# Optimization experiments

Hardware: AMD Instinct MI355X
Metric: run time of the kernel (lower is better)

## Reference

```python
import jax, jax.numpy as jnp
import numpy as np

FEAT_STRIDE = 16
PRE_NMS = 6000
POST_NMS = 300
NMS_THRESH = 0.7
NEG_THR = 0.3
POS_THR = 0.7
RPN_BATCH = 256
FG_FRAC = 0.5
SCALES = (8, 16, 32)
RATIOS = (0.5, 1.0, 2.0)
A = len(SCALES) * len(RATIOS)  # 9


def _generate_anchors():
    base = 16.0
    ctr = (base - 1.0) * 0.5
    size = base * base
    out = []
    for r in RATIOS:
        ws = np.round(np.sqrt(size / r))
        hs = np.round(ws * r)
        for s in SCALES:
            W = ws * s
            H = hs * s
            out.append([ctr - 0.5 * (W - 1), ctr - 0.5 * (H - 1),
                        ctr + 0.5 * (W - 1), ctr + 0.5 * (H - 1)])
    return np.array(out, np.float32)  # [9,4]


def _conv(x, w, b, pad):
    y = jax.lax.conv_general_dilated(x, w, (1, 1), [(pad, pad), (pad, pad)],
                                     dimension_numbers=('NCHW', 'OIHW', 'NCHW'))
    return y + b[None, :, None, None]


def _all_anchors(H, W):
    base = jnp.asarray(_generate_anchors())
    sx = jnp.arange(W, dtype=jnp.float32) * FEAT_STRIDE
    sy = jnp.arange(H, dtype=jnp.float32) * FEAT_STRIDE
    gy, gx = jnp.meshgrid(sy, sx, indexing='ij')
    shifts = jnp.stack([gx, gy, gx, gy], -1).reshape(-1, 1, 4)  # [H*W,1,4]
    return (shifts + base[None]).reshape(-1, 4)  # (h,w,a) order, [H*W*A,4]


def _decode(anchors, deltas):
    w = anchors[:, 2] - anchors[:, 0] + 1.0
    h = anchors[:, 3] - anchors[:, 1] + 1.0
    cx = anchors[:, 0] + 0.5 * w
    cy = anchors[:, 1] + 0.5 * h
    pcx = deltas[:, 0] * w + cx
    pcy = deltas[:, 1] * h + cy
    pw = jnp.exp(deltas[:, 2]) * w
    ph = jnp.exp(deltas[:, 3]) * h
    return jnp.stack([pcx - 0.5 * pw, pcy - 0.5 * ph, pcx + 0.5 * pw, pcy + 0.5 * ph], -1)


def _encode(anchors, gt):
    ew = anchors[:, 2] - anchors[:, 0] + 1.0
    eh = anchors[:, 3] - anchors[:, 1] + 1.0
    ecx = anchors[:, 0] + 0.5 * ew
    ecy = anchors[:, 1] + 0.5 * eh
    gw = gt[:, 2] - gt[:, 0] + 1.0
    gh = gt[:, 3] - gt[:, 1] + 1.0
    gcx = gt[:, 0] + 0.5 * gw
    gcy = gt[:, 1] + 0.5 * gh
    return jnp.stack([(gcx - ecx) / ew, (gcy - ecy) / eh,
                      jnp.log(gw / ew), jnp.log(gh / eh)], -1)


def _nms(boxes, scores, thresh, max_out):
    x1, y1, x2, y2 = boxes[:, 0], boxes[:, 1], boxes[:, 2], boxes[:, 3]
    areas = (x2 - x1 + 1.0) * (y2 - y1 + 1.0)
    N = boxes.shape[0]

    def body(k, st):
        valid, sel, selv = st
        s = jnp.where(valid, scores, -jnp.inf)
        i = jnp.argmax(s)
        ok = s[i] > -jnp.inf
        iw = jnp.maximum(jnp.minimum(x2[i], x2) - jnp.maximum(x1[i], x1) + 1.0, 0.0)
        ih = jnp.maximum(jnp.minimum(y2[i], y2) - jnp.maximum(y1[i], y1) + 1.0, 0.0)
        inter = iw * ih
        iou = inter / (areas[i] + areas - inter)
        valid = valid & (iou <= thresh)
        return valid, sel.at[k].set(i.astype(jnp.int32)), selv.at[k].set(ok)

    st = jax.lax.fori_loop(0, max_out, body,
                           (jnp.ones(N, bool), jnp.zeros(max_out, jnp.int32), jnp.zeros(max_out, bool)))
    return st[1], st[2]


def _propose_one(scores, deltas, anchors, imh, imw):
    boxes = _decode(anchors, deltas)
    boxes = jnp.stack([jnp.clip(boxes[:, 0], 0.0, imw - 1.0),
                       jnp.clip(boxes[:, 1], 0.0, imh - 1.0),
                       jnp.clip(boxes[:, 2], 0.0, imw - 1.0),
                       jnp.clip(boxes[:, 3], 0.0, imh - 1.0)], -1)
    top_s, idx = jax.lax.top_k(scores, PRE_NMS)
    top_b = boxes[idx]
    sel, selv = _nms(top_b, top_s, NMS_THRESH, POST_NMS)
    return top_b[sel] * selv[:, None].astype(top_b.dtype)  # [POST_NMS,4], zero rows when exhausted


def _anchor_target_one(gt, imh, imw, rfg, rbg, anchors):
    N = anchors.shape[0]
    ax1, ay1, ax2, ay2 = anchors[:, 0], anchors[:, 1], anchors[:, 2], anchors[:, 3]
    inside = (ax1 >= 0) & (ay1 >= 0) & (ax2 < imw) & (ay2 < imh)
    gx1, gy1, gx2, gy2 = gt[:, 0], gt[:, 1], gt[:, 2], gt[:, 3]
    gw = gx2 - gx1 + 1.0
    gh = gy2 - gy1 + 1.0
    gt_valid = ~((gw == 1.0) & (gh == 1.0))  # all-zero padded gt boxes
    aw = ax2 - ax1 + 1.0
    ah = ay2 - ay1 + 1.0
    iw = jnp.maximum(jnp.minimum(ax2[:, None], gx2[None, :]) - jnp.maximum(ax1[:, None], gx1[None, :]) + 1.0, 0.0)
    ih = jnp.maximum(jnp.minimum(ay2[:, None], gy2[None, :]) - jnp.maximum(ay1[:, None], gy1[None, :]) + 1.0, 0.0)
    inter = iw * ih
    iou = inter / ((aw * ah)[:, None] + (gw * gh)[None, :] - inter)  # [N,K]
    iou = jnp.where(gt_valid[None, :], iou, 0.0)
    iou = jnp.where(inside[:, None], iou, -1.0)  # outside anchors excluded, as in original
    max_ov = iou.max(1)
    arg = iou.argmax(1)
    gt_max = iou.max(0)
    gt_max = jnp.where(gt_max <= 0.0, 1e-5, gt_max)
    keep = (iou == gt_max[None, :]).any(1)  # anchors with max overlap per gt -> fg
    labels = jnp.full(N, -1.0, jnp.float32)
    labels = jnp.where(max_ov < NEG_THR, 0.0, labels)
    labels = jnp.where(keep, 1.0, labels)
    labels = jnp.where(max_ov >= POS_THR, 1.0, labels)
    labels = jnp.where(inside, labels, -1.0)

    def ranks(r, mask):
        order = jnp.argsort(jnp.where(mask, r, 2.0))
        return jnp.zeros(N, jnp.int32).at[order].set(jnp.arange(N, dtype=jnp.int32))

    num_fg = int(FG_FRAC * RPN_BATCH)
    fg_keep = (labels == 1.0) & (ranks(rfg, labels == 1.0) < num_fg)
    num_bg = RPN_BATCH - fg_keep.sum()
    bg_keep = (labels == 0.0) & (ranks(rbg, labels == 0.0) < num_bg)
    labels = jnp.where(fg_keep, 1.0, jnp.where(bg_keep, 0.0, -1.0))
    targets = _encode(anchors, gt[arg, :4])
    ones4 = jnp.ones((1, 4), jnp.float32)
    in_w = (labels == 1.0).astype(jnp.float32)[:, None] * ones4
    n_ex = (labels >= 0).sum().astype(jnp.float32)
    out_w = jnp.where(labels >= 0, 1.0 / n_ex, 0.0)[:, None] * ones4
    return labels, targets, in_w, out_w


def _rpn_forward(base_feat, im_info, gt_boxes, conv_w, conv_b, cls_w, cls_b, bbox_w, bbox_b):
    B, _, H, W = base_feat.shape
    x = jax.nn.relu(_conv(base_feat, conv_w, conv_b, 1))
    cls_score = _conv(x, cls_w, cls_b, 0)                 # [B,2A,H,W]
    # reshape(x,2) -> softmax over axis 1 -> reshape back
    prob = jax.nn.softmax(cls_score.reshape(B, 2, A * H, W), axis=1).reshape(B, 2 * A, H, W)
    bbox_pred = _conv(x, bbox_w, bbox_b, 0)               # [B,4A,H,W]
    anchors = _all_anchors(H, W)                          # [H*W*A,4]

    # ---- proposal layer (detached in original) ----
    fg = prob[:, A:, :, :].transpose(0, 2, 3, 1).reshape(B, -1)        # (h,w,a)
    deltas = bbox_pred.transpose(0, 2, 3, 1).reshape(B, -1, 4)
    rois_boxes = jax.vmap(_propose_one, in_axes=(0, 0, None, 0, 0))(
        jax.lax.stop_gradient(fg), jax.lax.stop_gradient(deltas), anchors, im_info[:, 0], im_info[:, 1])
    batch_idx = jnp.broadcast_to(jnp.arange(B, dtype=rois_boxes.dtype)[:, None, None], (B, POST_NMS, 1))
    rois = jnp.concatenate([batch_idx, rois_boxes], -1)   # [B,POST_NMS,5]

    # ---- anchor target layer (training path) ----
    key = jax.random.key(42)
    rfg = jax.random.uniform(key, (B, anchors.shape[0]))
    rbg = jax.random.uniform(jax.random.fold_in(key, 1), (B, anchors.shape[0]))
    labels, targets, in_w, out_w = jax.vmap(_anchor_target_one, in_axes=(0, 0, 0, 0, 0, None))(
        gt_boxes, im_info[:, 0], im_info[:, 1], rfg, rbg, anchors)
    # rearrange (h,w,a) -> (a,h,w) layouts to match torch permutes
    labels = labels.reshape(B, H, W, A).transpose(0, 3, 1, 2).reshape(B, -1)
    targets = targets.reshape(B, H, W, A * 4).transpose(0, 3, 1, 2)
    in_w = in_w.reshape(B, H, W, A * 4).transpose(0, 3, 1, 2)
    out_w = out_w.reshape(B, H, W, A * 4).transpose(0, 3, 1, 2)

    # cross-entropy over kept anchors
    logits = cls_score.reshape(B, 2, A, H, W).transpose(0, 2, 3, 4, 1).reshape(-1, 2)
    lab = labels.reshape(-1)
    m = (lab >= 0).astype(logits.dtype)
    logp = jax.nn.log_softmax(logits, axis=-1)
    idx = jnp.clip(lab, 0.0, 1.0).astype(jnp.int32)
    nll = -jnp.take_along_axis(logp, idx[:, None], axis=1)[:, 0]
    loss_cls = (nll * m).sum() / m.sum()

    # smooth-L1 box loss, sigma=3, sum dims [1,2,3] then mean over batch
    sigma2 = 9.0
    diff = in_w * (bbox_pred - targets)
    ad = jnp.abs(diff)
    flag = (ad < 1.0 / sigma2).astype(diff.dtype)
    lb = flag * 0.5 * sigma2 * diff * diff + (1.0 - flag) * (ad - 0.5 / sigma2)
    loss_box = (out_w * lb).sum(axis=(1, 2, 3)).mean()
    return rois, loss_cls, loss_box


def setup_inputs() -> dict:
    key = jax.random.key(0)
    ks = jax.random.split(key, 9)
    B, C, H, W = 4, 512, 50, 76
    base_feat = jax.random.normal(ks[0], (B, C, H, W), jnp.float32)
    conv_w = jax.random.normal(ks[1], (512, C, 3, 3), jnp.float32) * 0.01
    conv_b = jnp.zeros((512,), jnp.float32)
    cls_w = jax.random.normal(ks[2], (18, 512, 1, 1), jnp.float32) * 0.01
    cls_b = jnp.zeros((18,), jnp.float32)
    bbox_w = jax.random.normal(ks[3], (36, 512, 1, 1), jnp.float32) * 0.01
    bbox_b = jnp.zeros((36,), jnp.float32)
    imh, imw = float(H * FEAT_STRIDE), float(W * FEAT_STRIDE)
    im_info = jnp.tile(jnp.array([imh, imw, 1.0], jnp.float32), (B, 1))
    K = 20
    cx = jax.random.uniform(ks[4], (B, K)) * (imw - 100.0) + 50.0
    cy = jax.random.uniform(ks[5], (B, K)) * (imh - 100.0) + 50.0
    bw = jax.random.uniform(ks[6], (B, K)) * 270.0 + 30.0
    bh = jax.random.uniform(ks[7], (B, K)) * 270.0 + 30.0
    x1 = jnp.clip(cx - 0.5 * bw, 0.0, imw - 1.0)
    x2 = jnp.clip(cx + 0.5 * bw, 0.0, imw - 1.0)
    y1 = jnp.clip(cy - 0.5 * bh, 0.0, imh - 1.0)
    y2 = jnp.clip(cy + 0.5 * bh, 0.0, imh - 1.0)
    cls = jax.random.randint(ks[8], (B, K), 1, 21).astype(jnp.float32)
    gt_boxes = jnp.stack([x1, y1, x2, y2, cls], -1)
    num_boxes = jnp.full((B,), K, jnp.int32)
    return {"base_feat": base_feat, "im_info": im_info, "gt_boxes": gt_boxes,
            "num_boxes": num_boxes, "conv_w": conv_w, "conv_b": conv_b,
            "cls_w": cls_w, "cls_b": cls_b, "bbox_w": bbox_w, "bbox_b": bbox_b}


def reference(base_feat, im_info, gt_boxes, num_boxes, conv_w, conv_b, cls_w, cls_b, bbox_w, bbox_b):
    # num_boxes is implicitly handled via zero-padded gt_boxes (as in the original layer)
    return _rpn_forward(base_feat, im_info, gt_boxes, conv_w, conv_b, cls_w, cls_b, bbox_w, bbox_b)
```

## Files before the change

### kernel.cpp

```cpp
#include <hip/hip_runtime.h>
#include <stdint.h>

#define HHH 50
#define WWW 76
#define NPIX 3800
#define NA 34200
#define PRE 6000
#define POST 300
#define NW 94
#define CIN 512
#define COUT 512
#define NBATCH 4
#define NGT 20
#define TFHALF 68400u
#define XTB 2252800

typedef __bf16 bf16x8 __attribute__((ext_vector_type(8)));
typedef float f32x4 __attribute__((ext_vector_type(4)));
typedef unsigned int u32x4v __attribute__((ext_vector_type(4)));

__device__ static inline f32x4 MFMA16(bf16x8 a, bf16x8 b, f32x4 c) {
  return __builtin_amdgcn_mfma_f32_16x16x32_bf16(a, b, c, 0, 0, 0);
}
__device__ static inline bf16x8 LD8(const unsigned short* p) {
  return __builtin_bit_cast(bf16x8, *(const u32x4v*)p);
}

__host__ __device__ static inline void tf2x32(unsigned k0, unsigned k1, unsigned& x0, unsigned& x1) {
  unsigned k2 = k0 ^ k1 ^ 0x1BD11BDAu;
#define TFR(r) do { x0 += x1; x1 = (x1 << (r)) | (x1 >> (32 - (r))); x1 ^= x0; } while (0)
  x0 += k0; x1 += k1;
  TFR(13); TFR(15); TFR(26); TFR(6);
  x0 += k1; x1 += k2 + 1u;
  TFR(17); TFR(29); TFR(16); TFR(24);
  x0 += k2; x1 += k0 + 2u;
  TFR(13); TFR(15); TFR(26); TFR(6);
  x0 += k0; x1 += k1 + 3u;
  TFR(17); TFR(29); TFR(16); TFR(24);
  x0 += k1; x1 += k2 + 4u;
  TFR(13); TFR(15); TFR(26); TFR(6);
  x0 += k2; x1 += k0 + 5u;
#undef TFR
}

__device__ static inline unsigned tf_u23(unsigned k0, unsigned k1, unsigned p) {
  unsigned x0, x1;
  if (p < TFHALF) { x0 = p; x1 = p + TFHALF; tf2x32(k0, k1, x0, x1); return x0 >> 9; }
  x0 = p - TFHALF; x1 = p; tf2x32(k0, k1, x0, x1); return x1 >> 9;
}

__device__ const float BA[9][4] = {
  {-84.f, -40.f,  99.f,  55.f}, {-176.f, -88.f, 191.f, 103.f}, {-360.f, -184.f, 375.f, 199.f},
  {-56.f, -56.f,  71.f,  71.f}, {-120.f, -120.f, 135.f, 135.f}, {-248.f, -248.f, 263.f, 263.f},
  {-36.f, -80.f,  51.f,  95.f}, {-80.f, -168.f,  95.f, 183.f}, {-168.f, -344.f, 183.f, 359.f}
};

__device__ static inline unsigned monoF(float f) {
  int b = __float_as_int(f);
  unsigned u = (unsigned)b;
  return (b < 0) ? ~u : (u | 0x80000000u);
}
__device__ static inline float unmonoF(unsigned u) {
  unsigned b = (u & 0x80000000u) ? (u ^ 0x80000000u) : ~u;
  return __int_as_float((int)b);
}

__device__ static inline void split3(float v, unsigned short& h, unsigned short& m, unsigned short& l) {
  __bf16 b0 = (__bf16)v;  float f0 = (float)b0;
  float r = v - f0;       __bf16 b1 = (__bf16)r;  float f1 = (float)b1;
  float r2 = r - f1;      __bf16 b2 = (__bf16)r2;
  h = __builtin_bit_cast(unsigned short, b0);
  m = __builtin_bit_cast(unsigned short, b1);
  l = __builtin_bit_cast(unsigned short, b2);
}

__global__ void k_split_x(const float* __restrict__ feat, unsigned short* __restrict__ x0,
                          unsigned short* __restrict__ x1, unsigned short* __restrict__ x2) {
  int tid = blockIdx.x * 256 + threadIdx.x;
  if (tid >= NBATCH * XTB) return;
  int b = tid / XTB;
  int rem = tid - b * XTB;
  int pg = rem >> 13;
  int r2 = rem & 8191;
  int cg = r2 >> 7;
  int po = (r2 >> 3) & 15;
  int cl = r2 & 7;
  int ci = cg * 8 + cl;
  int px = pg * 16 + po;
  int hq = px / 80, wq = px - hq * 80;
  float v = 0.f;
  if (hq >= 2 && hq < 52 && wq >= 1 && wq < 77)
    v = feat[((size_t)(b * 512 + ci)) * NPIX + (hq - 2) * 76 + (wq - 1)];
  unsigned short h, m, l;
  split3(v, h, m, l);
  x0[tid] = h; x1[tid] = m; x2[tid] = l;
}

__global__ void k_split_w(const float* __restrict__ cw, unsigned short* __restrict__ w0,
                          unsigned short* __restrict__ w1, unsigned short* __restrict__ w2,
                          unsigned* __restrict__ gtmaxU, int* __restrict__ cnts, float* __restrict__ accums) {
  int tid = blockIdx.x * 256 + threadIdx.x;
  if (blockIdx.x == 0) {
    int t = threadIdx.x;
    if (t < NBATCH * NGT) gtmaxU[t] = 0x407FFFFFu;
    if (t < 8) cnts[t] = 0;
    if (t < 8) accums[t] = 0.f;
  }
  if (tid >= 9 * 64 * 512 * 8) return;
  int cl = tid & 7;
  int co = (tid >> 3) & 511;
  int cg = (tid >> 12) & 63;
  int tap = tid >> 18;
  int ci = cg * 8 + cl;
  float v = cw[((size_t)co * 512 + ci) * 9 + tap];
  unsigned short h, m, l;
  split3(v, h, m, l);
  w0[tid] = h; w1[tid] = m; w2[tid] = l;
}

__global__ void k_tr_w1(const float* __restrict__ clsw, const float* __restrict__ bbw, float* __restrict__ wt1) {
  int tid = blockIdx.x * 256 + threadIdx.x;
  if (tid >= CIN * 64) return;
  int c = tid & 63, ci = tid >> 6;
  float v = 0.f;
  if (c < 18) v = clsw[c * 512 + ci];
  else if (c < 54) v = bbw[(c - 18) * 512 + ci];
  wt1[tid] = v;
}

__global__ __launch_bounds__(256, 2) void k_conv3(
    const unsigned short* __restrict__ XT0, const unsigned short* __restrict__ XT1,
    const unsigned short* __restrict__ XT2,
    const unsigned short* __restrict__ WT0, const unsigned short* __restrict__ WT1,
    const unsigned short* __restrict__ WT2,
    const float* __restrict__ bias, float* __restrict__ out) {
  const int d = blockIdx.x;
  const int copair = (d >> 1) & 3, half = d & 1, g = d >> 3;
  const int cob = copair * 2 + (g & 1);
  const int pxb = half * 64 + (g >> 1);
  const int pxp = pxb & 31, b = pxb >> 5;
  const int co0 = cob * 64;
  const int px0 = 160 + pxp * 128;
  const int t = threadIdx.x, l = t & 63, wv = t >> 6;
  const int wr = wv >> 1, wc = wv & 1;
  const int l15 = l & 15, lq = l >> 4;
  f32x4 cmain[2][4], ccorr[2][4];
  double accd[2][4][4];
#pragma unroll
  for (int c = 0; c < 2; ++c)
#pragma unroll
    for (int p = 0; p < 4; ++p) {
      cmain[c][p] = (f32x4)(0.f); ccorr[c][p] = (f32x4)(0.f);
#pragma unroll
      for (int r = 0; r < 4; ++r) accd[c][p][r] = 0.0;
    }
  const unsigned short* xt0 = XT0 + (size_t)b * XTB;
  const unsigned short* xt1 = XT1 + (size_t)b * XTB;
  const unsigned short* xt2 = XT2 + (size_t)b * XTB;
  const int coA = wr * 32 + l15;
  const int OFFT[9] = {-81, -80, -79, -1, 0, 1, 79, 80, 81};
  const int pxw = px0 + wc * 64 + l15;

  for (int kg = 0; kg < 16; ++kg) {
    const int cgl = kg * 4 + lq;
    const int cglo = cgl * 128;
    const size_t aro = ((size_t)cgl * 512 + co0 + coA) * 8;
#pragma unroll
    for (int tap = 0; tap < 9; ++tap) {
      const size_t ao = aro + (size_t)tap * (64 * 512 * 8);
      bf16x8 A0[2], A1[2], A2[2];
      A0[0] = LD8(WT0 + ao); A0[1] = LD8(WT0 + ao + 128);
      A1[0] = LD8(WT1 + ao); A1[1] = LD8(WT1 + ao + 128);
      A2[0] = LD8(WT2 + ao); A2[1] = LD8(WT2 + ao + 128);
      const int pxbase = pxw + OFFT[tap];
      const size_t eob = (size_t)((pxbase >> 4) * 8192 + (pxbase & 15) * 8 + cglo);
#pragma unroll
      for (int p = 0; p < 4; ++p) {
        const size_t eo = eob + (size_t)p * 8192;
        bf16x8 B0 = LD8(xt0 + eo);
        bf16x8 B1 = LD8(xt1 + eo);
        bf16x8 B2 = LD8(xt2 + eo);
#pragma unroll
        for (int c = 0; c < 2; ++c) {
          cmain[c][p] = MFMA16(A0[c], B0, cmain[c][p]);
          ccorr[c][p] = MFMA16(A2[c], B0, ccorr[c][p]);
          ccorr[c][p] = MFMA16(A0[c], B2, ccorr[c][p]);
          ccorr[c][p] = MFMA16(A1[c], B1, ccorr[c][p]);
          ccorr[c][p] = MFMA16(A1[c], B0, ccorr[c][p]);
          ccorr[c][p] = MFMA16(A0[c], B1, ccorr[c][p]);
        }
      }
    }
    if (kg & 1) {
#pragma unroll
      for (int c = 0; c < 2; ++c)
#pragma unroll
        for (int p = 0; p < 4; ++p) {
#pragma unroll
          for (int r = 0; r < 4; ++r) accd[c][p][r] += (double)cmain[c][p][r];
          cmain[c][p] = (f32x4)(0.f);
        }
    }
  }
  const size_t outb = ((size_t)b * 512 + co0) * NPIX;
#pragma unroll
  for (int c = 0; c < 2; ++c)
#pragma unroll
    for (int p = 0; p < 4; ++p)
#pragma unroll
      for (int r = 0; r < 4; ++r) {
        int coL = wr * 32 + c * 16 + lq * 4 + r;
        int px = px0 + wc * 64 + p * 16 + l15;
        int hq = px / 80, wq = px - hq * 80;
        if (hq >= 2 && hq < 52 && wq >= 1 && wq < 77) {
          float v = (float)(accd[c][p][r] + (double)ccorr[c][p][r]) + bias[co0 + coL];
          out[outb + (size_t)coL * NPIX + (hq - 2) * 76 + (wq - 1)] = fmaxf(v, 0.f);
        }
      }
}

__global__ __launch_bounds__(256) void k_conv1(const float* __restrict__ x, const float* __restrict__ wt1,
                                               const float* __restrict__ clsb, const float* __restrict__ bbb,
                                               float* __restrict__ clsS, float* __restrict__ bbp) {
  const int b = blockIdx.y;
  const int px0 = blockIdx.x * 128;
  const int t = threadIdx.x;
  const int cg = t & 7, pg = t >> 3;
  __shared__ float xs[16][128];
  __shared__ float ws[16][72];
  double acc[8][4];
#pragma unroll
  for (int i = 0; i < 8; ++i)
#pragma unroll
    for (int j = 0; j < 4; ++j) acc[i][j] = 0.0;
  const float* xb = x + (size_t)b * CIN * NPIX;
  for (int cc = 0; cc < CIN; cc += 16) {
#pragma unroll
    for (int e0 = 0; e0 < 8; ++e0) {
      int e = t + e0 * 256;
      int r = e >> 7, c = e & 127;
      int p = px0 + c;
      xs[r][c] = (p < NPIX) ? xb[(size_t)(cc + r) * NPIX + p] : 0.f;
    }
#pragma unroll
    for (int e0 = 0; e0 < 4; ++e0) {
      int e = t + e0 * 256;
      int r = e >> 6, c = e & 63;
      ws[r][c + ((c >> 5) << 2)] = wt1[(cc + r) * 64 + c];
    }
    __syncthreads();
    const int wcol = (cg << 3) + ((cg >> 2) << 2);
    const int xcol = pg << 2;
    float a32[8][4];
#pragma unroll
    for (int i = 0; i < 8; ++i)
#pragma unroll
      for (int j = 0; j < 4; ++j) a32[i][j] = 0.f;
#pragma unroll
    for (int k = 0; k < 16; ++k) {
      const float4 w0 = *(const float4*)&ws[k][wcol];
      const float4 w1 = *(const float4*)&ws[k][wcol + 4];
      const float4 xa = *(const float4*)&xs[k][xcol];
      const float wv[8] = {w0.x, w0.y, w0.z, w0.w, w1.x, w1.y, w1.z, w1.w};
      const float xv[4] = {xa.x, xa.y, xa.z, xa.w};
#pragma unroll
      for (int i = 0; i < 8; ++i)
#pragma unroll
        for (int j = 0; j < 4; ++j)
          a32[i][j] = fmaf(wv[i], xv[j], a32[i][j]);
    }
#pragma unroll
    for (int i = 0; i < 8; ++i)
#pragma unroll
      for (int j = 0; j < 4; ++j) acc[i][j] += (double)a32[i][j];
    __syncthreads();
  }
#pragma unroll
  for (int i = 0; i < 8; ++i) {
    int c = cg * 8 + i;
#pragma unroll
    for (int j = 0; j < 4; ++j) {
      int p = px0 + pg * 4 + j;
      if (p < NPIX) {
        if (c < 18) clsS[((size_t)b * 18 + c) * NPIX + p] = (float)acc[i][j] + clsb[c];
        else if (c < 54) bbp[((size_t)b * 36 + (c - 18)) * NPIX + p] = (float)acc[i][j] + bbb[c - 18];
      }
    }
  }
}

__global__ void k_decode(const float* __restrict__ clsS, const float* __restrict__ bbp,
                         const float* __restrict__ im_info, float* __restrict__ boxes,
                         unsigned long long* __restrict__ keys) {
  int tid = blockIdx.x * 256 + threadIdx.x;
  int b = tid >> 16, n = tid & 0xFFFF;
  if (n >= NA) return;
  int a = n % 9, p = n / 9;
  int h = p / WWW, w = p - h * WWW;
  const float* cb = clsS + (size_t)b * 18 * NPIX;
  float s0 = cb[(size_t)a * NPIX + p];
  float s1 = cb[(size_t)(9 + a) * NPIX + p];
  float mx = fmaxf(s0, s1);
  float e0 = expf(s0 - mx), e1 = expf(s1 - mx);
  float fg = e1 / (e0 + e1);
  const float* bb = bbp + (size_t)b * 36 * NPIX;
  float d0 = bb[(size_t)(a * 4 + 0) * NPIX + p];
  float d1 = bb[(size_t)(a * 4 + 1) * NPIX + p];
  float d2 = bb[(size_t)(a * 4 + 2) * NPIX + p];
  float d3 = bb[(size_t)(a * 4 + 3) * NPIX + p];
  float ax1 = BA[a][0] + w * 16.f, ay1 = BA[a][1] + h * 16.f;
  float ax2 = BA[a][2] + w * 16.f, ay2 = BA[a][3] + h * 16.f;
  float aw = ax2 - ax1 + 1.f, ah = ay2 - ay1 + 1.f;
  float acx = ax1 + 0.5f * aw, acy = ay1 + 0.5f * ah;
  float pcx = d0 * aw + acx, pcy = d1 * ah + acy;
  float pw = expf(d2) * aw, ph = expf(d3) * ah;
  float imh = im_info[b * 3 + 0], imw = im_info[b * 3 + 1];
  float x1 = fminf(fmaxf(pcx - 0.5f * pw, 0.f), imw - 1.f);
  float y1 = fminf(fmaxf(pcy - 0.5f * ph, 0.f), imh - 1.f);
  float x2 = fminf(fmaxf(pcx + 0.5f * pw, 0.f), imw - 1.f);
  float y2 = fminf(fmaxf(pcy + 0.5f * ph, 0.f), imh - 1.f);
  float* bx = boxes + ((size_t)b * NA + n) * 4;
  bx[0] = x1; bx[1] = y1; bx[2] = x2; bx[3] = y2;
  unsigned fb = __float_as_uint(fg);
  keys[((size_t)b << 16) + n] = ((unsigned long long)fb << 32) | (unsigned)(~(unsigned)n);
}

__global__ __launch_bounds__(1024) void k_rsel_top(const unsigned long long* __restrict__ keys,
                                                   unsigned long long* __restrict__ comp) {
  const int b = blockIdx.x;
  const unsigned long long* kb = keys + ((size_t)b << 16);
  __shared__ int hist[16][256];
  __shared__ int histT[256];
  __shared__ unsigned long long sh_prefix;
  __shared__ unsigned sh_r;
  __shared__ int sh_cnt;
  const int t = threadIdx.x, wid = t >> 6, lane = t & 63;
  if (t == 0) { sh_prefix = 0ull; sh_r = PRE; sh_cnt = 0; }
  __syncthreads();
  for (int p = 5; p >= 0; --p) {
    for (int e = t; e < 4096; e += 1024) ((int*)hist)[e] = 0;
    __syncthreads();
    unsigned long long pref = sh_prefix;
    for (int i = t; i < NA; i += 1024) {
      unsigned long long k = kb[i];
      unsigned long long k48 = ((k >> 16) & 0xFFFFFFFF0000ull) | (k & 0xFFFFull);
      bool m = (p == 5) || ((k48 >> (8 * (p + 1))) == pref);
      unsigned bucket = (unsigned)((k48 >> (8 * p)) & 255);
      unsigned long long act = __ballot(m);
      while (act) {
        int src = __ffsll(act) - 1;
        unsigned v0 = __shfl(bucket, src);
        unsigned long long same = __ballot(m && (bucket == v0));
        if (lane == src) atomicAdd(&hist[wid][v0], (int)__popcll(same));
        act &= ~same;
      }
    }
    __syncthreads();
    if (t < 256) { int s = 0; for (int w = 0; w < 16; ++w) s += hist[w][t]; histT[t] = s; }
    __syncthreads();
    if (t == 0) {
      unsigned rr = sh_r; unsigned cum = 0;
      for (int v = 255; v >= 0; --v) {
        cum += (unsigned)histT[v];
        if (cum >= rr) { sh_r = rr - (cum - (unsigned)histT[v]); sh_prefix = (sh_prefix << 8) | (unsigned)v; break; }
      }
    }
    __syncthreads();
  }
  const unsigned long long thr48 = sh_prefix;
  for (int base = 0; base < NA; base += 1024) {
    int i = base + t;
    bool keep = false;
    unsigned long long k = 0ull;
    if (i < NA) {
      k = kb[i];
      unsigned long long k48 = ((k >> 16) & 0xFFFFFFFF0000ull) | (k & 0xFFFFull);
      keep = (k48 >= thr48);
    }
    unsigned long long bal = __ballot(keep);
    if (bal) {
      int leader = __ffsll(bal) - 1;
      int basepos = 0;
      if (lane == leader) basepos = atomicAdd(&sh_cnt, (int)__popcll(bal));
      basepos = __shfl(basepos, leader);
      if (keep) {
        int off = __popcll(bal & ((1ull << lane) - 1ull));
        comp[b * 8192 + basepos + off] = k;
      }
    }
  }
}

__global__ __launch_bounds__(1024) void k_sort_lds(unsigned long long* __restrict__ comp) {
  __shared__ unsigned long long s[8192];
  const int b = blockIdx.x;
  const int t = threadIdx.x;
  unsigned long long* cb = comp + b * 8192;
  for (int e = t; e < 8192; e += 1024) s[e] = (e < PRE) ? cb[e] : 0ull;
  __syncthreads();
  for (int k = 2; k <= 8192; k <<= 1) {
    for (int j = k >> 1; j >= 1; j >>= 1) {
      for (int q = t; q < 4096; q += 1024) {
        int i = ((q & ~(j - 1)) << 1) | (q & (j - 1));
        int pp = i | j;
        bool up = (i & k) == 0;
        unsigned long long a = s[i], d = s[pp];
        if (up ? (a < d) : (a > d)) { s[i] = d; s[pp] = a; }
      }
      __syncthreads();
    }
  }
  for (int e = t; e < PRE; e += 1024) cb[e] = s[e];
}

__global__ void k_gather(const unsigned long long* __restrict__ comp, const float* __restrict__ boxes,
                         float* tbx1, float* tby1, float* tbx2, float* tby2, float* tba) {
  int tid = blockIdx.x * 256 + threadIdx.x;
  if (tid >= NBATCH * PRE) return;
  int b = tid / PRE;
  int k = tid - b * PRE;
  unsigned long long key = comp[b * 8192 + k];
  unsigned n = ~(unsigned)(key & 0xFFFFFFFFu);
  const float* bx = boxes + ((size_t)b * NA + n) * 4;
  float x1 = bx[0], y1 = bx[1], x2 = bx[2], y2 = bx[3];
  tbx1[tid] = x1; tby1[tid] = y1; tbx2[tid] = x2; tby2[tid] = y2;
  tba[tid] = (x2 - x1 + 1.f) * (y2 - y1 + 1.f);
}

__global__ __launch_bounds__(256) void k_mask(const float* __restrict__ tbx1, const float* __restrict__ tby1,
                                              const float* __restrict__ tbx2, const float* __restrict__ tby2,
                                              const float* __restrict__ tba, unsigned long long* __restrict__ mask) {
  const int b = blockIdx.y;
  const int i0 = blockIdx.x * 64;
  const int t = threadIdx.x;
  __shared__ float jx1[2048], jy1[2048], jx2[2048], jy2[2048], ja[2048];
  __shared__ float ix1[64], iy1[64], ix2[64], iy2[64], ia[64];
  const float* bx1 = tbx1 + b * PRE;
  const float* by1 = tby1 + b * PRE;
  const float* bx2 = tbx2 + b * PRE;
  const float* by2 = tby2 + b * PRE;
  const float* ba2 = tba + b * PRE;
  if (t < 64) {
    int i = i0 + t;
    if (i < PRE) { ix1[t] = bx1[i]; iy1[t] = by1[i]; ix2[t] = bx2[i]; iy2[t] = by2[i]; ia[t] = ba2[i]; }
    else { ix1[t] = 0; iy1[t] = 0; ix2[t] = 0; iy2[t] = 0; ia[t] = 1; }
  }
  for (int c = 0; c < 3; ++c) {
    int j0 = c * 2048;
    for (int e = t; e < 2048; e += 256) {
      int j = j0 + e;
      if (j < PRE) { jx1[e] = bx1[j]; jy1[e] = by1[j]; jx2[e] = bx2[j]; jy2[e] = by2[j]; ja[e] = ba2[j]; }
      else { jx1[e] = 0; jy1[e] = 0; jx2[e] = 0; jy2[e] = 0; ja[e] = 1; }
    }
    __syncthreads();
    for (int task = t; task < 64 * 32; task += 256) {
      int il = task & 63, wl = task >> 6;
      int i = i0 + il;
      int wg = (j0 >> 6) + wl;
      if (i >= PRE || wg >= NW) continue;
      unsigned long long word = 0ull;
      float X1 = ix1[il], Y1 = iy1[il], X2 = ix2[il], Y2 = iy2[il], A = ia[il];
      for (int l = 0; l < 64; ++l) {
        int j = wg * 64 + l;
        if (j > i && j < PRE) {
          int e = j - j0;
          float iw = fminf(X2, jx2[e]) - fmaxf(X1, jx1[e]) + 1.f;
          float ih = fminf(Y2, jy2[e]) - fmaxf(Y1, jy1[e]) + 1.f;
          if (iw > 0.f && ih > 0.f) {
            float inter = iw * ih;
            float iou = inter / (A + ja[e] - inter);
            if (iou > 0.7f) word |= (1ull << l);
          }
        }
      }
      mask[((size_t)(b * PRE + i)) * NW + wg] = word;
    }
    __syncthreads();
  }
}

__global__ void k_nms(const unsigned long long* __restrict__ mask,
                      const float* __restrict__ tbx1, const float* __restrict__ tby1,
                      const float* __restrict__ tbx2, const float* __restrict__ tby2,
                      float* __restrict__ out) {
  const int b = blockIdx.x;
  const int lane = threadIdx.x;
  unsigned long long rem0 = 0ull;
  unsigned long long rem1;
  if (64 + lane < NW) rem1 = (64 + lane == NW - 1) ? ~((1ull << (PRE - (NW - 1) * 64)) - 1ull) : 0ull;
  else rem1 = ~0ull;
  int sc = 0;
  for (; sc < POST; ++sc) {
    unsigned long long a0 = ~rem0, a1 = ~rem1;
    unsigned long long bal0 = __ballot(a0 != 0ull);
    int w, l;
    if (bal0) {
      int src = __ffsll(bal0) - 1;
      unsigned long long av = __shfl(a0, src);
      w = src; l = __ffsll(av) - 1;
    } else {
      unsigned long long bal1 = __ballot(a1 != 0ull);
      if (!bal1) break;
      int src = __ffsll(bal1) - 1;
      unsigned long long av = __shfl(a1, src);
      w = 64 + src; l = __ffsll(av) - 1;
    }
    int j = w * 64 + l;
    if (lane < 5) {
      float v;
      if (lane == 0) v = (float)b;
      else if (lane == 1) v = tbx1[b * PRE + j];
      else if (lane == 2) v = tby1[b * PRE + j];
      else if (lane == 3) v = tbx2[b * PRE + j];
      else v = tby2[b * PRE + j];
      out[((size_t)(b * POST + sc)) * 5 + lane] = v;
    }
    const unsigned long long* row = mask + ((size_t)(b * PRE + j)) * NW;
    rem0 |= row[lane];
    if (64 + lane < NW) rem1 |= row[64 + lane];
    if (w < 64) { if (lane == w) rem0 |= (1ull << l); }
    else if (lane == w - 64) rem1 |= (1ull << l);
  }
  for (int r2 = sc; r2 < POST; ++r2)
    if (lane < 5) out[((size_t)(b * POST + r2)) * 5 + lane] = (lane == 0) ? (float)b : 0.f;
}

__global__ __launch_bounds__(256) void k_iouA(const float* __restrict__ gt_boxes, const float* __restrict__ im_info,
                                              float* __restrict__ iou, float* __restrict__ maxov,
                                              int* __restrict__ argm, unsigned* __restrict__ gtmaxU) {
  const int b = blockIdx.y;
  const int n = blockIdx.x * 256 + threadIdx.x;
  __shared__ float g[NGT][6];
  if (threadIdx.x < NGT) {
    const float* gg = gt_boxes + (b * NGT + threadIdx.x) * 5;
    float x1 = gg[0], y1 = gg[1], x2 = gg[2], y2 = gg[3];
    g[threadIdx.x][0] = x1; g[threadIdx.x][1] = y1; g[threadIdx.x][2] = x2; g[threadIdx.x][3] = y2;
    float gw = x2 - x1 + 1.f, gh = y2 - y1 + 1.f;
    g[threadIdx.x][4] = gw * gh;
    g[threadIdx.x][5] = ((gw == 1.f) && (gh == 1.f)) ? 0.f : 1.f;
  }
  __syncthreads();
  if (n >= NA) return;
  int a = n % 9, p = n / 9;
  int h = p / WWW, w = p - h * WWW;
  float ax1 = BA[a][0] + w * 16.f, ay1 = BA[a][1] + h * 16.f;
  float ax2 = BA[a][2] + w * 16.f, ay2 = BA[a][3] + h * 16.f;
  float imh = im_info[b * 3 + 0], imw = im_info[b * 3 + 1];
  bool inside = (ax1 >= 0.f) && (ay1 >= 0.f) && (ax2 < imw) && (ay2 < imh);
  float aw = ax2 - ax1 + 1.f, ah = ay2 - ay1 + 1.f;
  float aa = aw * ah;
  float best = -2.f;
  int barg = 0;
  float* row = iou + ((size_t)(b * NA) + n) * NGT;
#pragma unroll
  for (int j = 0; j < NGT; ++j) {
    float iw = fmaxf(fminf(ax2, g[j][2]) - fmaxf(ax1, g[j][0]) + 1.f, 0.f);
    float ih = fmaxf(fminf(ay2, g[j][3]) - fmaxf(ay1, g[j][1]) + 1.f, 0.f);
    float inter = iw * ih;
    float v = inter / (aa + g[j][4] - inter);
    if (g[j][5] == 0.f) v = 0.f;
    if (!inside) v = -1.f;
    row[j] = v;
    if (v > best) { best = v; barg = j; }
    if (v > 0.f) atomicMax(&gtmaxU[b * NGT + j], monoF(v));
  }
  maxov[b * NA + n] = best;
  argm[b * NA + n] = barg;
}

__global__ __launch_bounds__(256) void k_labels(const float* __restrict__ iou, const float* __restrict__ maxov,
                                                const unsigned* __restrict__ gtmaxU, const float* __restrict__ im_info,
                                                unsigned kf0, unsigned kf1, unsigned kb0, unsigned kb1,
                                                int* __restrict__ labels, unsigned* __restrict__ ufg,
                                                unsigned* __restrict__ ubg, int* __restrict__ cnts) {
  const int b = blockIdx.y;
  const int n = blockIdx.x * 256 + threadIdx.x;
  __shared__ float gmf[NGT];
  if (threadIdx.x < NGT) {
    float gm = unmonoF(gtmaxU[b * NGT + threadIdx.x]);
    gmf[threadIdx.x] = (gm <= 0.f) ? 1e-5f : gm;
  }
  __syncthreads();
  int label = -1;
  if (n < NA) {
    int a = n % 9, p = n / 9;
    int h = p / WWW, w = p - h * WWW;
    float ax1 = BA[a][0] + w * 16.f, ay1 = BA[a][1] + h * 16.f;
    float ax2 = BA[a][2] + w * 16.f, ay2 = BA[a][3] + h * 16.f;
    float imh = im_info[b * 3 + 0], imw = im_info[b * 3 + 1];
    bool inside = (ax1 >= 0.f) && (ay1 >= 0.f) && (ax2 < imw) && (ay2 < imh);
    float mo = maxov[b * NA + n];
    const float* row = iou + ((size_t)(b * NA) + n) * NGT;
    bool keep = false;
#pragma unroll
    for (int j = 0; j < NGT; ++j) keep = keep || (row[j] == gmf[j]);
    if (mo < 0.3f) label = 0;
    if (keep) label = 1;
    if (mo >= 0.7f) label = 1;
    if (!inside) label = -1;
    labels[b * NA + n] = label;
    unsigned pp = (unsigned)(b * NA + n);
    ufg[b * NA + n] = (label == 1) ? tf_u23(kf0, kf1, pp) : 0x00FFFFFFu;
    ubg[b * NA + n] = (label == 0) ? tf_u23(kb0, kb1, pp) : 0x00FFFFFFu;
  }
  unsigned long long bf = __ballot(label == 1);
  unsigned long long bb = __ballot(label == 0);
  if ((threadIdx.x & 63) == 0) {
    atomicAdd(&cnts[b], (int)__popcll(bf));
    atomicAdd(&cnts[4 + b], (int)__popcll(bb));
  }
}

__global__ __launch_bounds__(1024) void k_rsel_samp(const unsigned* __restrict__ ufg, const unsigned* __restrict__ ubg,
                                                    const int* __restrict__ cnts, unsigned* __restrict__ selp,
                                                    float* __restrict__ nexf) {
  const int blk = blockIdx.x;
  const int b = blk >> 1, cls = blk & 1;
  const unsigned* u = (cls == 0 ? ufg : ubg) + (size_t)b * NA;
  const int fcnt = cnts[b], bcnt = cnts[4 + b];
  const int kk = (cls == 0) ? 128 : (256 - (fcnt < 128 ? fcnt : 128));
  const int cnt = (cls == 0) ? fcnt : bcnt;
  const int t = threadIdx.x, wid = t >> 6;
  __shared__ int hist[16][256];
  __shared__ int histT[256];
  __shared__ unsigned long long sh_prefix;
  __shared__ unsigned sh_r;
  if (t == 0) {
    if (cls == 1) {
      int fk = fcnt < 128 ? fcnt : 128;
      int bk2 = bcnt < kk ? bcnt : kk;
      nexf[b] = (float)(fk + bk2);
    }
    sh_prefix = 0ull; sh_r = (unsigned)kk;
  }
  __syncthreads();
  if (kk > cnt) {
    if (t == 0) { selp[blk * 2] = 0x00FFFFFFu; selp[blk * 2 + 1] = 0x1FFFFu; }
    return;
  }
  for (int p = 4; p >= 0; --p) {
    for (int e = t; e < 4096; e += 1024) ((int*)hist)[e] = 0;
    __syncthreads();
    unsigned long long pref = sh_prefix;
    for (int i = t; i < NA; i += 1024) {
      unsigned uv = u[i];
      if (uv == 0x00FFFFFFu) continue;
      unsigned long long k = ((unsigned long long)uv << 17) | (unsigned)i;
      if ((k >> (8 * (p + 1))) == pref)
        atomicAdd(&hist[wid][(int)((k >> (8 * p)) & 255)], 1);
    }
    __syncthreads();
    if (t < 256) { int s = 0; for (int w = 0; w < 16; ++w) s += hist[w][t]; histT[t] = s; }
    __syncthreads();
    if (t == 0) {
      unsigned rr = sh_r; unsigned cum = 0;
      for (int v = 0; v < 256; ++v) {
        cum += (unsigned)histT[v];
        if (cum >= rr) { sh_r = rr - (cum - (unsigned)histT[v]); sh_prefix = (sh_prefix << 8) | (unsigned)v; break; }
      }
    }
    __syncthreads();
  }
  if (t == 0) {
    selp[blk * 2] = (unsigned)(sh_prefix >> 17);
    selp[blk * 2 + 1] = (unsigned)(sh_prefix & 0x1FFFF);
  }
}

__global__ __launch_bounds__(256) void k_loss(const float* __restrict__ clsS, const float* __restrict__ bbp,
                                              const float* __restrict__ gt_boxes, const int* __restrict__ labels,
                                              const unsigned* __restrict__ ufg, const unsigned* __restrict__ ubg,
                                              const unsigned* __restrict__ selp, const int* __restrict__ argm,
                                              float* __restrict__ accums) {
  const int b = blockIdx.y;
  const int n = blockIdx.x * 256 + threadIdx.x;
  float nll = 0.f, mcnt = 0.f, lbsum = 0.f;
  if (n < NA) {
    int label = labels[b * NA + n];
    int fin = -1;
    if (label == 1) {
      unsigned uu = ufg[b * NA + n];
      unsigned thr = selp[(b * 2 + 0) * 2], ithr = selp[(b * 2 + 0) * 2 + 1];
      if (uu < thr || (uu == thr && (unsigned)n <= ithr)) fin = 1;
    } else if (label == 0) {
      unsigned uu = ubg[b * NA + n];
      unsigned thr = selp[(b * 2 + 1) * 2], ithr = selp[(b * 2 + 1) * 2 + 1];
      if (uu < thr || (uu == thr && (unsigned)n <= ithr)) fin = 0;
    }
    if (fin >= 0) {
      int a = n % 9, p = n / 9;
      float s0 = clsS[((size_t)b * 18 + a) * NPIX + p];
      float s1 = clsS[((size_t)b * 18 + 9 + a) * NPIX + p];
      float mx = fmaxf(s0, s1);
      float lse = mx + logf(expf(s0 - mx) + expf(s1 - mx));
      nll = lse - (fin == 1 ? s1 : s0);
      mcnt = 1.f;
      if (fin == 1) {
        int h = p / WWW, w = p - h * WWW;
        float ax1 = BA[a][0] + w * 16.f, ay1 = BA[a][1] + h * 16.f;
        float ax2 = BA[a][2] + w * 16.f, ay2 = BA[a][3] + h * 16.f;
        float ew = ax2 - ax1 + 1.f, eh = ay2 - ay1 + 1.f;
        float ecx = ax1 + 0.5f * ew, ecy = ay1 + 0.5f * eh;
        int ag = argm[b * NA + n];
        const float* gg = gt_boxes + (b * NGT + ag) * 5;
        float gw = gg[2] - gg[0] + 1.f, gh = gg[3] - gg[1] + 1.f;
        float gcx = gg[0] + 0.5f * gw, gcy = gg[1] + 0.5f * gh;
        float tt[4];
        tt[0] = (gcx - ecx) / ew;
        tt[1] = (gcy - ecy) / eh;
        tt[2] = logf(gw / ew);
        tt[3] = logf(gh / eh);
#pragma unroll
        for (int dd = 0; dd < 4; ++dd) {
          float pd = bbp[((size_t)b * 36 + (a * 4 + dd)) * NPIX + p];
          float diff = pd - tt[dd];
          float ad = fabsf(diff);
          lbsum += (ad < 1.f / 9.f) ? 4.5f * diff * diff : (ad - 0.5f / 9.f);
        }
      }
    }
  }
  for (int o = 32; o > 0; o >>= 1) {
    nll += __shfl_down(nll, o);
    mcnt += __shfl_down(mcnt, o);
    lbsum += __shfl_down(lbsum, o);
  }
  __shared__ float p0[4], p1[4], p2[4];
  int wid = threadIdx.x >> 6;
  if ((threadIdx.x & 63) == 0) { p0[wid] = nll; p1[wid] = mcnt; p2[wid] = lbsum; }
  __syncthreads();
  if (threadIdx.x == 0) {
    float aS = 0, bS = 0, cS = 0;
    for (int q = 0; q < 4; ++q) { aS += p0[q]; bS += p1[q]; cS += p2[q]; }
    atomicAdd(&accums[0], aS);
    atomicAdd(&accums[1], bS);
    atomicAdd(&accums[2 + b], cS);
  }
}

__global__ void k_final(const float* __restrict__ accums, const float* __restrict__ nexf, float* __restrict__ out) {
  if (threadIdx.x == 0 && blockIdx.x == 0) {
    out[6000] = accums[0] / accums[1];
    float lb = 0.f;
    for (int b = 0; b < NBATCH; ++b) lb += accums[2 + b] / nexf[b];
    out[6001] = lb * 0.25f;
  }
}

extern "C" void kernel_launch(void* const* d_in, const int* in_sizes, int n_in,
                              void* d_out, int out_size, void* d_ws, size_t ws_size,
                              hipStream_t stream) {
  (void)in_sizes; (void)n_in; (void)out_size; (void)ws_size;
  const float* base_feat = (const float*)d_in[0];
  const float* im_info   = (const float*)d_in[1];
  const float* gt_boxes  = (const float*)d_in[2];
  const float* conv_w    = (const float*)d_in[4];
  const float* conv_b    = (const float*)d_in[5];
  const float* cls_w     = (const float*)d_in[6];
  const float* cls_b     = (const float*)d_in[7];
  const float* bbox_w    = (const float*)d_in[8];
  const float* bbox_b    = (const float*)d_in[9];
  float* out = (float*)d_out;

  char* wp = (char*)d_ws;
  auto carve = [&](size_t bytes) -> void* {
    void* r = (void*)wp;
    wp += (bytes + 255) & ~(size_t)255;
    return r;
  };
  float* x     = (float*)carve((size_t)NBATCH * CIN * NPIX * 4);
  float* clsS  = (float*)carve((size_t)NBATCH * 18 * NPIX * 4);
  float* bbp   = (float*)carve((size_t)NBATCH * 36 * NPIX * 4);
  unsigned short* WT0 = (unsigned short*)carve((size_t)9 * 64 * 512 * 8 * 2);
  unsigned short* WT1 = (unsigned short*)carve((size_t)9 * 64 * 512 * 8 * 2);
  unsigned short* WT2 = (unsigned short*)carve((size_t)9 * 64 * 512 * 8 * 2);
  float* wt1   = (float*)carve((size_t)CIN * 64 * 4);
  unsigned* gtmaxU = (unsigned*)carve(NBATCH * NGT * 4);
  int* cnts    = (int*)carve(8 * 4);
  unsigned* selp = (unsigned*)carve(16 * 4);
  float* nexf  = (float*)carve(4 * 4);
  float* accums = (float*)carve(8 * 4);

  char* overlay = wp;
  unsigned short* XT0 = (unsigned short*)overlay;
  unsigned short* XT1 = XT0 + (size_t)NBATCH * XTB;
  unsigned short* XT2 = XT1 + (size_t)NBATCH * XTB;
  char* wp2 = overlay;
  auto carve2 = [&](size_t bytes) -> void* {
    void* r = (void*)wp2;
    wp2 += (bytes + 255) & ~(size_t)255;
    return r;
  };
  float* boxes = (float*)carve2((size_t)NBATCH * NA * 4 * 4);
  unsigned long long* keys = (unsigned long long*)carve2((size_t)NBATCH * 65536 * 8);
  float* tbx1 = (float*)carve2((size_t)NBATCH * PRE * 4);
  float* tby1 = (float*)carve2((size_t)NBATCH * PRE * 4);
  float* tbx2 = (float*)carve2((size_t)NBATCH * PRE * 4);
  float* tby2 = (float*)carve2((size_t)NBATCH * PRE * 4);
  float* tba  = (float*)carve2((size_t)NBATCH * PRE * 4);
  unsigned long long* mask = (unsigned long long*)carve2((size_t)NBATCH * PRE * NW * 8);
  float* iou   = (float*)carve2((size_t)NBATCH * NA * NGT * 4);
  float* maxov = (float*)carve2((size_t)NBATCH * NA * 4);
  int* argm    = (int*)carve2((size_t)NBATCH * NA * 4);
  int* labels  = (int*)carve2((size_t)NBATCH * NA * 4);
  unsigned* ufg = (unsigned*)carve2((size_t)NBATCH * NA * 4);
  unsigned* ubg = (unsigned*)carve2((size_t)NBATCH * NA * 4);
  unsigned long long* comp = (unsigned long long*)carve2((size_t)NBATCH * 8192 * 8);

  unsigned kb0 = 0u, kb1 = 1u;
  tf2x32(0u, 42u, kb0, kb1);

  k_split_w<<<dim3((9 * 64 * 512 * 8) / 256), dim3(256), 0, stream>>>(conv_w, WT0, WT1, WT2, gtmaxU, cnts, accums);
  k_tr_w1<<<dim3((CIN * 64) / 256), dim3(256), 0, stream>>>(cls_w, bbox_w, wt1);
  k_split_x<<<dim3((NBATCH * XTB + 255) / 256), dim3(256), 0, stream>>>(base_feat, XT0, XT1, XT2);
  k_conv3<<<dim3(1024), dim3(256), 0, stream>>>(XT0, XT1, XT2, WT0, WT1, WT2, conv_b, x);
  k_conv1<<<dim3(30, 4), dim3(256), 0, stream>>>(x, wt1, cls_b, bbox_b, clsS, bbp);
  k_decode<<<dim3(NBATCH * 65536 / 256), dim3(256), 0, stream>>>(clsS, bbp, im_info, boxes, keys);
  k_rsel_top<<<dim3(NBATCH), dim3(1024), 0, stream>>>(keys, comp);
  k_sort_lds<<<dim3(NBATCH), dim3(1024), 0, stream>>>(comp);
  k_gather<<<dim3((NBATCH * PRE + 255) / 256), dim3(256), 0, stream>>>(comp, boxes, tbx1, tby1, tbx2, tby2, tba);
  k_mask<<<dim3(NW, NBATCH), dim3(256), 0, stream>>>(tbx1, tby1, tbx2, tby2, tba, mask);
  k_nms<<<dim3(NBATCH), dim3(64), 0, stream>>>(mask, tbx1, tby1, tbx2, tby2, out);
  k_iouA<<<dim3((NA + 255) / 256, NBATCH), dim3(256), 0, stream>>>(gt_boxes, im_info, iou, maxov, argm, gtmaxU);
  k_labels<<<dim3((NA + 255) / 256, NBATCH), dim3(256), 0, stream>>>(iou, maxov, gtmaxU, im_info,
                                                                     0u, 42u, kb0, kb1, labels, ufg, ubg, cnts);
  k_rsel_samp<<<dim3(8), dim3(1024), 0, stream>>>(ufg, ubg, cnts, selp, nexf);
  k_loss<<<dim3((NA + 255) / 256, NBATCH), dim3(256), 0, stream>>>(clsS, bbp, gt_boxes, labels, ufg, ubg, selp, argm, accums);
  k_final<<<dim3(1), dim3(1), 0, stream>>>(accums, nexf, out);
}
```

Baseline: 1.517 ms.

## Drop fp64 conv accumulation, fuse gather into sort, reduce IoU atomics

The conv3 kernel replaces its per-two-K-group double-precision accumulation with an fp32 master accumulator updated every K group, which removes the fp64 conversion and add work and frees registers. The radix-select histogram drops the ballot-and-match loop in favour of plain per-element LDS atomics. The separate gather kernel is merged into the LDS sort kernel, saving one launch and a global round-trip of the sorted keys. The IoU kernel reduces per-gt maxima across each wave with shuffles before issuing one global atomicMax per gt per block. The fp32 accumulation may slightly change numerics near the thresholds.

```diff
diff --git a/kernel.cpp b/kernel.cpp
--- a/kernel.cpp
+++ b/kernel.cpp
@@ -144,15 +144,12 @@
   const int t = threadIdx.x, l = t & 63, wv = t >> 6;
   const int wr = wv >> 1, wc = wv & 1;
   const int l15 = l & 15, lq = l >> 4;
-  f32x4 cmain[2][4], ccorr[2][4];
-  double accd[2][4][4];
+  f32x4 cmain[2][4], ccorr[2][4], cmast[2][4];
 #pragma unroll
   for (int c = 0; c < 2; ++c)
 #pragma unroll
     for (int p = 0; p < 4; ++p) {
-      cmain[c][p] = (f32x4)(0.f); ccorr[c][p] = (f32x4)(0.f);
-#pragma unroll
-      for (int r = 0; r < 4; ++r) accd[c][p][r] = 0.0;
+      cmain[c][p] = (f32x4)(0.f); ccorr[c][p] = (f32x4)(0.f); cmast[c][p] = (f32x4)(0.f);
     }
   const unsigned short* xt0 = XT0 + (size_t)b * XTB;
   const unsigned short* xt1 = XT1 + (size_t)b * XTB;
@@ -191,16 +188,13 @@
         }
       }
     }
-    if (kg & 1) {
-#pragma unroll
-      for (int c = 0; c < 2; ++c)
-#pragma unroll
-        for (int p = 0; p < 4; ++p) {
-#pragma unroll
-          for (int r = 0; r < 4; ++r) accd[c][p][r] += (double)cmain[c][p][r];
-          cmain[c][p] = (f32x4)(0.f);
-        }
-    }
+#pragma unroll
+    for (int c = 0; c < 2; ++c)
+#pragma unroll
+      for (int p = 0; p < 4; ++p) {
+        cmast[c][p] += cmain[c][p];
+        cmain[c][p] = (f32x4)(0.f);
+      }
   }
   const size_t outb = ((size_t)b * 512 + co0) * NPIX;
 #pragma unroll
@@ -213,7 +207,7 @@
         int px = px0 + wc * 64 + p * 16 + l15;
         int hq = px / 80, wq = px - hq * 80;
         if (hq >= 2 && hq < 52 && wq >= 1 && wq < 77) {
-          float v = (float)(accd[c][p][r] + (double)ccorr[c][p][r]) + bias[co0 + coL];
+          float v = (cmast[c][p][r] + ccorr[c][p][r]) + bias[co0 + coL];
           out[outb + (size_t)coL * NPIX + (hq - 2) * 76 + (wq - 1)] = fmaxf(v, 0.f);
         }
       }
@@ -345,15 +339,7 @@
       unsigned long long k = kb[i];
       unsigned long long k48 = ((k >> 16) & 0xFFFFFFFF0000ull) | (k & 0xFFFFull);
       bool m = (p == 5) || ((k48 >> (8 * (p + 1))) == pref);
-      unsigned bucket = (unsigned)((k48 >> (8 * p)) & 255);
-      unsigned long long act = __ballot(m);
-      while (act) {
-        int src = __ffsll(act) - 1;
-        unsigned v0 = __shfl(bucket, src);
-        unsigned long long same = __ballot(m && (bucket == v0));
-        if (lane == src) atomicAdd(&hist[wid][v0], (int)__popcll(same));
-        act &= ~same;
-      }
+      if (m) atomicAdd(&hist[wid][(int)((k48 >> (8 * p)) & 255)], 1);
     }
     __syncthreads();
     if (t < 256) { int s = 0; for (int w = 0; w < 16; ++w) s += hist[w][t]; histT[t] = s; }
@@ -391,11 +377,15 @@
   }
 }
 
-__global__ __launch_bounds__(1024) void k_sort_lds(unsigned long long* __restrict__ comp) {
+__global__ __launch_bounds__(1024) void k_sort_lds(const unsigned long long* __restrict__ comp,
+                                                   const float* __restrict__ boxes,
+                                                   float* __restrict__ tbx1, float* __restrict__ tby1,
+                                                   float* __restrict__ tbx2, float* __restrict__ tby2,
+                                                   float* __restrict__ tba) {
   __shared__ unsigned long long s[8192];
   const int b = blockIdx.x;
   const int t = threadIdx.x;
-  unsigned long long* cb = comp + b * 8192;
+  const unsigned long long* cb = comp + b * 8192;
   for (int e = t; e < 8192; e += 1024) s[e] = (e < PRE) ? cb[e] : 0ull;
   __syncthreads();
   for (int k = 2; k <= 8192; k <<= 1) {
@@ -410,21 +400,15 @@
       __syncthreads();
     }
   }
-  for (int e = t; e < PRE; e += 1024) cb[e] = s[e];
-}
-
-__global__ void k_gather(const unsigned long long* __restrict__ comp, const float* __restrict__ boxes,
-                         float* tbx1, float* tby1, float* tbx2, float* tby2, float* tba) {
-  int tid = blockIdx.x * 256 + threadIdx.x;
-  if (tid >= NBATCH * PRE) return;
-  int b = tid / PRE;
-  int k = tid - b * PRE;
-  unsigned long long key = comp[b * 8192 + k];
-  unsigned n = ~(unsigned)(key & 0xFFFFFFFFu);
-  const float* bx = boxes + ((size_t)b * NA + n) * 4;
-  float x1 = bx[0], y1 = bx[1], x2 = bx[2], y2 = bx[3];
-  tbx1[tid] = x1; tby1[tid] = y1; tbx2[tid] = x2; tby2[tid] = y2;
-  tba[tid] = (x2 - x1 + 1.f) * (y2 - y1 + 1.f);
+  for (int e = t; e < PRE; e += 1024) {
+    unsigned long long key = s[e];
+    unsigned n = ~(unsigned)(key & 0xFFFFFFFFu);
+    const float* bx = boxes + ((size_t)b * NA + n) * 4;
+    float x1 = bx[0], y1 = bx[1], x2 = bx[2], y2 = bx[3];
+    int o = b * PRE + e;
+    tbx1[o] = x1; tby1[o] = y1; tbx2[o] = x2; tby2[o] = y2;
+    tba[o] = (x2 - x1 + 1.f) * (y2 - y1 + 1.f);
+  }
 }
 
 __global__ __launch_bounds__(256) void k_mask(const float* __restrict__ tbx1, const float* __restrict__ tby1,
@@ -530,42 +514,61 @@
                                               int* __restrict__ argm, unsigned* __restrict__ gtmaxU) {
   const int b = blockIdx.y;
   const int n = blockIdx.x * 256 + threadIdx.x;
+  const int t = threadIdx.x, lane = t & 63, wv = t >> 6;
   __shared__ float g[NGT][6];
-  if (threadIdx.x < NGT) {
-    const float* gg = gt_boxes + (b * NGT + threadIdx.x) * 5;
+  __shared__ float wmax[4][NGT];
+  if (t < NGT) {
+    const float* gg = gt_boxes + (b * NGT + t) * 5;
     float x1 = gg[0], y1 = gg[1], x2 = gg[2], y2 = gg[3];
-    g[threadIdx.x][0] = x1; g[threadIdx.x][1] = y1; g[threadIdx.x][2] = x2; g[threadIdx.x][3] = y2;
+    g[t][0] = x1; g[t][1] = y1; g[t][2] = x2; g[t][3] = y2;
     float gw = x2 - x1 + 1.f, gh = y2 - y1 + 1.f;
-    g[threadIdx.x][4] = gw * gh;
-    g[threadIdx.x][5] = ((gw == 1.f) && (gh == 1.f)) ? 0.f : 1.f;
+    g[t][4] = gw * gh;
+    g[t][5] = ((gw == 1.f) && (gh == 1.f)) ? 0.f : 1.f;
   }
   __syncthreads();
-  if (n >= NA) return;
-  int a = n % 9, p = n / 9;
-  int h = p / WWW, w = p - h * WWW;
-  float ax1 = BA[a][0] + w * 16.f, ay1 = BA[a][1] + h * 16.f;
-  float ax2 = BA[a][2] + w * 16.f, ay2 = BA[a][3] + h * 16.f;
-  float imh = im_info[b * 3 + 0], imw = im_info[b * 3 + 1];
-  bool inside = (ax1 >= 0.f) && (ay1 >= 0.f) && (ax2 < imw) && (ay2 < imh);
-  float aw = ax2 - ax1 + 1.f, ah = ay2 - ay1 + 1.f;
-  float aa = aw * ah;
+  const bool act = (n < NA);
+  float vj[NGT];
   float best = -2.f;
   int barg = 0;
-  float* row = iou + ((size_t)(b * NA) + n) * NGT;
+  if (act) {
+    int a = n % 9, p = n / 9;
+    int h = p / WWW, w = p - h * WWW;
+    float ax1 = BA[a][0] + w * 16.f, ay1 = BA[a][1] + h * 16.f;
+    float ax2 = BA[a][2] + w * 16.f, ay2 = BA[a][3] + h * 16.f;
+    float imh = im_info[b * 3 + 0], imw = im_info[b * 3 + 1];
+    bool inside = (ax1 >= 0.f) && (ay1 >= 0.f) && (ax2 < imw) && (ay2 < imh);
+    float aw = ax2 - ax1 + 1.f, ah = ay2 - ay1 + 1.f;
+    float aa = aw * ah;
+    float* row = iou + ((size_t)(b * NA) + n) * NGT;
+#pragma unroll
+    for (int j = 0; j < NGT; ++j) {
+      float iw = fmaxf(fminf(ax2, g[j][2]) - fmaxf(ax1, g[j][0]) + 1.f, 0.f);
+      float ih = fmaxf(fminf(ay2, g[j][3]) - fmaxf(ay1, g[j][1]) + 1.f, 0.f);
+      float inter = iw * ih;
+      float v = inter / (aa + g[j][4] - inter);
+      if (g[j][5] == 0.f) v = 0.f;
+      if (!inside) v = -1.f;
+      row[j] = v;
+      vj[j] = v;
+      if (v > best) { best = v; barg = j; }
+    }
+    maxov[b * NA + n] = best;
+    argm[b * NA + n] = barg;
+  } else {
+#pragma unroll
+    for (int j = 0; j < NGT; ++j) vj[j] = -1.f;
+  }
 #pragma unroll
   for (int j = 0; j < NGT; ++j) {
-    float iw = fmaxf(fminf(ax2, g[j][2]) - fmaxf(ax1, g[j][0]) + 1.f, 0.f);
-    float ih = fmaxf(fminf(ay2, g[j][3]) - fmaxf(ay1, g[j][1]) + 1.f, 0.f);
-    float inter = iw * ih;
-    float v = inter / (aa + g[j][4] - inter);
-    if (g[j][5] == 0.f) v = 0.f;
-    if (!inside) v = -1.f;
-    row[j] = v;
-    if (v > best) { best = v; barg = j; }
-    if (v > 0.f) atomicMax(&gtmaxU[b * NGT + j], monoF(v));
-  }
-  maxov[b * NA + n] = best;
-  argm[b * NA + n] = barg;
+    float red = vj[j];
+    for (int o = 32; o > 0; o >>= 1) red = fmaxf(red, __shfl_xor(red, o));
+    if (lane == 0) wmax[wv][j] = red;
+  }
+  __syncthreads();
+  if (t < NGT) {
+    float m = fmaxf(fmaxf(wmax[0][t], wmax[1][t]), fmaxf(wmax[2][t], wmax[3][t]));
+    if (m > 0.f) atomicMax(&gtmaxU[b * NGT + t], monoF(m));
+  }
 }
 
 __global__ __launch_bounds__(256) void k_labels(const float* __restrict__ iou, const float* __restrict__ maxov,
@@ -817,8 +820,7 @@
   k_conv1<<<dim3(30, 4), dim3(256), 0, stream>>>(x, wt1, cls_b, bbox_b, clsS, bbp);
   k_decode<<<dim3(NBATCH * 65536 / 256), dim3(256), 0, stream>>>(clsS, bbp, im_info, boxes, keys);
   k_rsel_top<<<dim3(NBATCH), dim3(1024), 0, stream>>>(keys, comp);
-  k_sort_lds<<<dim3(NBATCH), dim3(1024), 0, stream>>>(comp);
-  k_gather<<<dim3((NBATCH * PRE + 255) / 256), dim3(256), 0, stream>>>(comp, boxes, tbx1, tby1, tbx2, tby2, tba);
+  k_sort_lds<<<dim3(NBATCH), dim3(1024), 0, stream>>>(comp, boxes, tbx1, tby1, tbx2, tby2, tba);
   k_mask<<<dim3(NW, NBATCH), dim3(256), 0, stream>>>(tbx1, tby1, tbx2, tby2, tba, mask);
   k_nms<<<dim3(NBATCH), dim3(64), 0, stream>>>(mask, tbx1, tby1, tbx2, tby2, out);
   k_iouA<<<dim3((NA + 255) / 256, NBATCH), dim3(256), 0, stream>>>(gt_boxes, im_info, iou, maxov, argm, gtmaxU);
```

Result: slower. 1.643 ms (+8.4%).
